# Optimization experiments

Hardware: AMD Instinct MI355X
Metric: run time of the kernel (lower is better)

The kernel has to match this reference:

```python
import jax, jax.numpy as jnp
import numpy as np

N = 100_000      # nodes
E = 1_600_000    # edges (avg degree 16)
F_IN = 128       # dataset.num_features
H = 128          # hidden
C = 25_000       # num_clusters (~ target_ratio 0.25 * N)
G = 64           # graphs in batch
NCLS = 10        # dataset.num_classes


def _gcn_conv(x, w, b, src, dst, n):
    # PyG GCNConv: add self loops, symmetric normalization deg^-1/2 A_hat deg^-1/2
    h = x @ w  # [n, out]
    deg = jnp.zeros((n,), x.dtype).at[dst].add(1.0) + 1.0  # +1 self loop
    dis = jax.lax.rsqrt(deg)
    norm = dis[src] * dis[dst]  # [E]
    out = jnp.zeros_like(h).at[dst].add(h[src] * norm[:, None])
    out = out + h * (dis * dis)[:, None]  # self-loop term norm_ii = deg_i^-1
    return out + b


def _mean_pool(x, seg, num_seg):
    s = jax.ops.segment_sum(x, seg, num_segments=num_seg)
    cnt = jax.ops.segment_sum(jnp.ones((x.shape[0],), x.dtype), seg, num_segments=num_seg)
    return s / jnp.maximum(cnt, 1.0)[:, None]


def _max_pool(x, seg, num_seg):
    m = jax.ops.segment_max(x, seg, num_segments=num_seg)
    cnt = jax.ops.segment_sum(jnp.ones((x.shape[0],), x.dtype), seg, num_segments=num_seg)
    return jnp.where(cnt[:, None] > 0, m, 0.0)


def setup_inputs() -> dict:
    key = jax.random.key(0)
    ks = jax.random.split(key, 12)
    def glorot(k, shape):
        fan_in = shape[0]
        return (jax.random.normal(k, shape, jnp.float32) / np.sqrt(fan_in)).astype(jnp.float32)
    return {
        "x": jax.random.normal(ks[0], (N, F_IN), jnp.float32),
        "edge_index": jax.random.randint(ks[1], (2, E), 0, N, dtype=jnp.int32).astype(jnp.int64),
        "batch": jnp.sort(jax.random.randint(ks[2], (N,), 0, G, dtype=jnp.int32)).astype(jnp.int64),
        "cluster": jax.random.randint(ks[3], (N,), 0, C, dtype=jnp.int32).astype(jnp.int64),
        "num_clusters": C,
        "num_graphs": G,
        "W1": glorot(ks[4], (F_IN, H)), "b1": jnp.zeros((H,), jnp.float32),
        "W2": glorot(ks[5], (H, H)),   "b2": jnp.zeros((H,), jnp.float32),
        "W3": glorot(ks[6], (H, H)),   "b3": jnp.zeros((H,), jnp.float32),
        "lin1_w": glorot(ks[7], (4 * H, H)), "lin1_b": jnp.zeros((H,), jnp.float32),
        "lin2_w": glorot(ks[8], (H, NCLS)),  "lin2_b": jnp.zeros((NCLS,), jnp.float32),
    }


def reference(x, edge_index, batch, cluster, num_clusters, num_graphs,
              W1, b1, W2, b2, W3, b3, lin1_w, lin1_b, lin2_w, lin2_b):
    n = x.shape[0]
    src, dst = edge_index[0], edge_index[1]
    # conv1 + relu (dropout is identity in eval mode)
    h = jax.nn.relu(_gcn_conv(x, W1, b1, src, dst, n))
    pre_mean = _mean_pool(h, batch, num_graphs)
    pre_max = _max_pool(h, batch, num_graphs)
    # LaCorePooling(aggregate='mean'): segment-mean nodes by cluster id,
    # relabel edges to cluster ids, derive pooled batch vector.
    hp = _mean_pool(h, cluster, num_clusters)            # [C, H]
    src_p, dst_p = cluster[src], cluster[dst]            # pooled edge list
    batch_p = jax.ops.segment_max(batch, cluster, num_segments=num_clusters)
    batch_p = jnp.maximum(batch_p, 0)                    # empty clusters -> graph 0
    # post-pool GCN layers
    hp = jax.nn.relu(_gcn_conv(hp, W2, b2, src_p, dst_p, num_clusters))
    hp = jax.nn.relu(_gcn_conv(hp, W3, b3, src_p, dst_p, num_clusters))
    post_mean = _mean_pool(hp, batch_p, num_graphs)
    post_max = _max_pool(hp, batch_p, num_graphs)
    z = jnp.concatenate([pre_mean, pre_max, post_mean, post_max], axis=-1)  # [G, 4H]
    z = jax.nn.relu(z @ lin1_w + lin1_b)
    z = z @ lin2_w + lin2_b
    return jax.nn.log_softmax(z, axis=-1)
```

## Files before the change

kernel.cpp:

```cpp
#include <hip/hip_runtime.h>

constexpr int N_NODES = 100000;
constexpr int N_EDGES = 1600000;
constexpr int N_CLUST = 25000;
constexpr int N_GRAPH = 64;
constexpr int NCLSN   = 10;

constexpr int BKT1_SHIFT = 9;
constexpr int NBKT1 = (N_NODES + 511) / 512;
constexpr int BKT2_SHIFT = 7;
constexpr int NBKT2 = (N_CLUST + 127) / 128;
constexpr int EPB = 4096;
constexpr int NEB = (N_EDGES + EPB - 1) / EPB;
constexpr int SORT_CAP = 12288;

constexpr int SCAN_BPB = 1024;
constexpr int NB1 = (N_NODES + SCAN_BPB - 1) / SCAN_BPB;
constexpr int NB2 = (N_CLUST + SCAN_BPB - 1) / SCAN_BPB;
constexpr int NB3 = (N_CLUST + SCAN_BPB - 1) / SCAN_BPB;
constexpr int NBT = NB1 + NB2 + NB3;

__device__ __forceinline__ float bf16lo(unsigned u){ return __uint_as_float(u << 16); }
__device__ __forceinline__ float bf16hi(unsigned u){ return __uint_as_float(u & 0xffff0000u); }
__device__ __forceinline__ unsigned bf16_rne(float f){
  unsigned u = __float_as_uint(f);
  return (u + 0x7fffu + ((u >> 16) & 1u)) >> 16;
}
__device__ __forceinline__ unsigned pack2(float lo, float hi){
  return bf16_rne(lo) | (bf16_rne(hi) << 16);
}

typedef short bf16x8 __attribute__((ext_vector_type(8)));
typedef float f32x4  __attribute__((ext_vector_type(4)));

__launch_bounds__(256)
__global__ void count_kernel(const int* __restrict__ ei, const int* __restrict__ cluster,
                             int* __restrict__ gcnt1, int* __restrict__ gcnt2){
  __shared__ int h1c[NBKT1], h2c[NBKT2];
  int t = threadIdx.x;
  for (int i = t; i < NBKT1; i += 256) h1c[i] = 0;
  for (int i = t; i < NBKT2; i += 256) h2c[i] = 0;
  __syncthreads();
  int e0 = blockIdx.x * EPB;
  #pragma unroll
  for (int i = 0; i < EPB / 256; ++i){
    int e = e0 + i * 256 + t;
    if (e < N_EDGES){
      int dst = ei[N_EDGES + e];
      int cd  = cluster[dst];
      atomicAdd(&h1c[dst >> BKT1_SHIFT], 1);
      atomicAdd(&h2c[cd  >> BKT2_SHIFT], 1);
    }
  }
  __syncthreads();
  for (int i = t; i < NBKT1; i += 256) if (h1c[i]) atomicAdd(&gcnt1[i], h1c[i]);
  for (int i = t; i < NBKT2; i += 256) if (h2c[i]) atomicAdd(&gcnt2[i], h2c[i]);
}

__launch_bounds__(256)
__global__ void bucket_scan(const int* __restrict__ gcnt1, const int* __restrict__ gcnt2,
                            int* __restrict__ gbase1, int* __restrict__ gcur1,
                            int* __restrict__ gbase2, int* __restrict__ gcur2){
  __shared__ int s[256];
  int t = threadIdx.x;
  int v = (t < NBKT1) ? gcnt1[t] : 0;
  s[t] = v; __syncthreads();
  for (int off = 1; off < 256; off <<= 1){
    int a = (t >= off) ? s[t - off] : 0;
    __syncthreads(); s[t] += a; __syncthreads();
  }
  if (t < NBKT1){ gbase1[t] = s[t] - v; gcur1[t] = s[t] - v; }
  __syncthreads();
  v = (t < NBKT2) ? gcnt2[t] : 0;
  s[t] = v; __syncthreads();
  for (int off = 1; off < 256; off <<= 1){
    int a = (t >= off) ? s[t - off] : 0;
    __syncthreads(); s[t] += a; __syncthreads();
  }
  if (t < NBKT2){ gbase2[t] = s[t] - v; gcur2[t] = s[t] - v; }
}

__launch_bounds__(256)
__global__ void scatter_kernel(const int* __restrict__ ei, const int* __restrict__ cluster,
                               int* __restrict__ gcur1, int* __restrict__ gcur2,
                               unsigned int* __restrict__ stage1, unsigned int* __restrict__ stage2){
  __shared__ int h1c[NBKT1], h2c[NBKT2];
  __shared__ int gb1[NBKT1], gb2[NBKT2];
  int t = threadIdx.x;
  for (int i = t; i < NBKT1; i += 256) h1c[i] = 0;
  for (int i = t; i < NBKT2; i += 256) h2c[i] = 0;
  __syncthreads();
  int e0 = blockIdx.x * EPB;
  #pragma unroll
  for (int i = 0; i < EPB / 256; ++i){
    int e = e0 + i * 256 + t;
    if (e < N_EDGES){
      int dst = ei[N_EDGES + e];
      int cd  = cluster[dst];
      atomicAdd(&h1c[dst >> BKT1_SHIFT], 1);
      atomicAdd(&h2c[cd  >> BKT2_SHIFT], 1);
    }
  }
  __syncthreads();
  for (int i = t; i < NBKT1; i += 256){ int c = h1c[i]; gb1[i] = c ? atomicAdd(&gcur1[i], c) : 0; }
  for (int i = t; i < NBKT2; i += 256){ int c = h2c[i]; gb2[i] = c ? atomicAdd(&gcur2[i], c) : 0; }
  __syncthreads();
  for (int i = t; i < NBKT1; i += 256) h1c[i] = 0;
  for (int i = t; i < NBKT2; i += 256) h2c[i] = 0;
  __syncthreads();
  #pragma unroll
  for (int i = 0; i < EPB / 256; ++i){
    int e = e0 + i * 256 + t;
    if (e < N_EDGES){
      int src = ei[e], dst = ei[N_EDGES + e];
      int cs = cluster[src], cd = cluster[dst];
      int b1 = dst >> BKT1_SHIFT, b2 = cd >> BKT2_SHIFT;
      int r1 = atomicAdd(&h1c[b1], 1);
      int r2 = atomicAdd(&h2c[b2], 1);
      stage1[gb1[b1] + r1] = ((unsigned)(dst & 511) << 17) | (unsigned)src;
      stage2[gb2[b2] + r2] = ((unsigned)(cd & 127) << 15) | (unsigned)cs;
    }
  }
}

template<int NBINS, int PSHIFT>
__launch_bounds__(256)
__global__ void bucket_sort(const unsigned int* __restrict__ stage, const int* __restrict__ gbase,
                            const int* __restrict__ gcnt, int* __restrict__ outpay,
                            int* __restrict__ deg, int ntot){
  __shared__ int cnt[NBINS], off[NBINS];
  __shared__ int sorted[SORT_CAP];
  int b = blockIdx.x, t = threadIdx.x;
  int base = gbase[b], n = gcnt[b];
  for (int i = t; i < NBINS; i += 256) cnt[i] = 0;
  __syncthreads();
  for (int i = t; i < n; i += 256) atomicAdd(&cnt[stage[base + i] >> PSHIFT], 1);
  __syncthreads();
  for (int i = t; i < NBINS; i += 256){
    int idx = b * NBINS + i;
    if (idx < ntot) deg[idx] = cnt[i];
    off[i] = cnt[i];
  }
  __syncthreads();
  for (int s = 1; s < NBINS; s <<= 1){
    int v0 = 0, v1 = 0;
    if (t < NBINS && t >= s) v0 = off[t - s];
    if (NBINS > 256 && t + 256 < NBINS && t + 256 >= s) v1 = off[t + 256 - s];
    __syncthreads();
    if (t < NBINS) off[t] += v0;
    if (NBINS > 256 && t + 256 < NBINS) off[t + 256] += v1;
    __syncthreads();
  }
  for (int i = t; i < NBINS; i += 256) off[i] -= cnt[i];
  __syncthreads();
  constexpr unsigned PMASK = (1u << PSHIFT) - 1u;
  if (n <= SORT_CAP){
    for (int i = t; i < n; i += 256){
      unsigned w = stage[base + i];
      int r = atomicAdd(&off[w >> PSHIFT], 1);
      sorted[r] = (int)(w & PMASK);
    }
    __syncthreads();
    for (int i = t; i < n; i += 256) outpay[base + i] = sorted[i];
  } else {
    for (int i = t; i < n; i += 256){
      unsigned w = stage[base + i];
      int r = atomicAdd(&off[w >> PSHIFT], 1);
      outpay[base + r] = (int)(w & PMASK);
    }
  }
}

__global__ void cntn_kernel(const int* __restrict__ cluster, int* __restrict__ cntn){
  int v = blockIdx.x * blockDim.x + threadIdx.x;
  if (v < N_NODES) atomicAdd(&cntn[cluster[v]], 1);
}

__device__ __forceinline__ void seg_select(int b, const int* deg1, const int* cntn,
                                           const int* deg2, const int*& src, int& n, int& base){
  if (b < NB1){ src = deg1; n = N_NODES; base = b * SCAN_BPB; }
  else if (b < NB1 + NB2){ src = cntn; n = N_CLUST; base = (b - NB1) * SCAN_BPB; }
  else { src = deg2; n = N_CLUST; base = (b - NB1 - NB2) * SCAN_BPB; }
}

__launch_bounds__(256)
__global__ void block_sums(const int* __restrict__ deg1, const int* __restrict__ cntn,
                           const int* __restrict__ deg2, int* __restrict__ bsum){
  int b = blockIdx.x;
  const int* src; int n, base;
  seg_select(b, deg1, cntn, deg2, src, n, base);
  int t = threadIdx.x;
  int i0 = base + t * 4;
  int s = 0;
  if (i0 + 3 < n){ int4 v = *(const int4*)&src[i0]; s = v.x + v.y + v.z + v.w; }
  else { for (int j = 0; j < 4; ++j){ int i = i0 + j; if (i < n) s += src[i]; } }
  __shared__ int sh[256];
  sh[t] = s; __syncthreads();
  for (int off = 128; off > 0; off >>= 1){
    if (t < off) sh[t] += sh[t + off];
    __syncthreads();
  }
  if (t == 0) bsum[b] = sh[0];
}

__launch_bounds__(256)
__global__ void scan_bsums(const int* __restrict__ bsum, int* __restrict__ boff,
                           int* __restrict__ rowptr1, int* __restrict__ rowptrn,
                           int* __restrict__ rowptr2){
  __shared__ int s[256];
  int t = threadIdx.x;
  int v = (t < NBT) ? bsum[t] : 0;
  s[t] = v; __syncthreads();
  int seg = (t < NB1) ? 0 : (t < NB1 + NB2 ? 1 : 2);
  for (int off = 1; off < 256; off <<= 1){
    int add = 0;
    if (t >= off){
      int u = t - off;
      int useg = (u < NB1) ? 0 : (u < NB1 + NB2 ? 1 : 2);
      if (useg == seg) add = s[u];
    }
    __syncthreads();
    s[t] += add;
    __syncthreads();
  }
  if (t < NBT) boff[t] = s[t] - v;
  if (t == NB1 - 1)       rowptr1[N_NODES] = s[t];
  if (t == NB1 + NB2 - 1) rowptrn[N_CLUST] = s[t];
  if (t == NBT - 1)       rowptr2[N_CLUST] = s[t];
}

__launch_bounds__(256)
__global__ void scan_final(const int* __restrict__ deg1, const int* __restrict__ cntn,
                           const int* __restrict__ deg2, const int* __restrict__ boff,
                           int* __restrict__ rowptr1, float* __restrict__ dis1,
                           int* __restrict__ rowptrn, int* __restrict__ curn,
                           int* __restrict__ rowptr2, float* __restrict__ dis2){
  int b = blockIdx.x;
  const int* src; int n, base;
  seg_select(b, deg1, cntn, deg2, src, n, base);
  int* rp; int* cur; float* dis;
  if (b < NB1){ rp = rowptr1; cur = nullptr; dis = dis1; }
  else if (b < NB1 + NB2){ rp = rowptrn; cur = curn; dis = nullptr; }
  else { rp = rowptr2; cur = nullptr; dis = dis2; }
  int t = threadIdx.x;
  int i0 = base + t * 4;
  int v[4]; int s = 0;
  #pragma unroll
  for (int j = 0; j < 4; ++j){ int i = i0 + j; v[j] = (i < n) ? src[i] : 0; s += v[j]; }
  __shared__ int sh[256];
  sh[t] = s; __syncthreads();
  for (int off = 1; off < 256; off <<= 1){
    int add = (t >= off) ? sh[t - off] : 0;
    __syncthreads();
    sh[t] += add;
    __syncthreads();
  }
  int run = sh[t] - s + boff[b];
  #pragma unroll
  for (int j = 0; j < 4; ++j){
    int i = i0 + j;
    if (i < n){
      rp[i] = run;
      if (cur) cur[i] = run;
      if (dis) dis[i] = rsqrtf((float)v[j] + 1.0f);
      run += v[j];
    }
  }
}

__global__ void fill_n(const int* __restrict__ cluster, int* __restrict__ curn,
                       int* __restrict__ nidx){
  int v = blockIdx.x * blockDim.x + threadIdx.x;
  if (v >= N_NODES) return;
  nidx[atomicAdd(&curn[cluster[v]], 1)] = v;
}

template<bool A_BF16>
__launch_bounds__(256)
__global__ void gemm_mfma(const void* __restrict__ Aptr, const float* __restrict__ B,
                          const float* __restrict__ scale, unsigned* __restrict__ Cmat,
                          int M){
  __shared__ __align__(16) unsigned Blds[128 * 68];
  __shared__ __align__(16) unsigned Alds[64 * 68];
  const int t = threadIdx.x;
  const int row0 = blockIdx.x * 64;

  #pragma unroll
  for (int i = 0; i < 8; ++i){
    int task = t + i * 256;
    int kp = task >> 5, nq = task & 31;
    float4 b0 = *(const float4*)&B[(2 * kp) * 128 + nq * 4];
    float4 b1 = *(const float4*)&B[(2 * kp + 1) * 128 + nq * 4];
    Blds[(nq * 4 + 0) * 68 + kp] = pack2(b0.x, b1.x);
    Blds[(nq * 4 + 1) * 68 + kp] = pack2(b0.y, b1.y);
    Blds[(nq * 4 + 2) * 68 + kp] = pack2(b0.z, b1.z);
    Blds[(nq * 4 + 3) * 68 + kp] = pack2(b0.w, b1.w);
  }
  if (A_BF16){
    const unsigned* A = (const unsigned*)Aptr;
    #pragma unroll
    for (int i = 0; i < 8; ++i){
      int idx = t + i * 256;
      int row = idx >> 5, c2 = idx & 31;
      int grow = min(row0 + row, M - 1);
      uint2 v = *(const uint2*)&A[(size_t)grow * 64 + c2 * 2];
      Alds[row * 68 + c2 * 2]     = v.x;
      Alds[row * 68 + c2 * 2 + 1] = v.y;
    }
  } else {
    const float* A = (const float*)Aptr;
    #pragma unroll
    for (int i = 0; i < 8; ++i){
      int idx = t + i * 256;
      int row = idx >> 5, k4 = idx & 31;
      int grow = min(row0 + row, M - 1);
      float4 v = *(const float4*)&A[(size_t)grow * 128 + k4 * 4];
      Alds[row * 68 + k4 * 2]     = pack2(v.x, v.y);
      Alds[row * 68 + k4 * 2 + 1] = pack2(v.z, v.w);
    }
  }
  __syncthreads();

  const int wv = t >> 6, l = t & 63, quad = l >> 4, n16 = l & 15;
  f32x4 acc[8];
  #pragma unroll
  for (int nt = 0; nt < 8; ++nt) acc[nt] = (f32x4){0.f, 0.f, 0.f, 0.f};
  const int arow = wv * 16 + n16;
  #pragma unroll
  for (int ks = 0; ks < 4; ++ks){
    bf16x8 af = *(const bf16x8*)&Alds[arow * 68 + ks * 16 + quad * 4];
    #pragma unroll
    for (int nt = 0; nt < 8; ++nt){
      bf16x8 bfr = *(const bf16x8*)&Blds[(nt * 16 + n16) * 68 + ks * 16 + quad * 4];
      acc[nt] = __builtin_amdgcn_mfma_f32_16x16x32_bf16(af, bfr, acc[nt], 0, 0, 0);
    }
  }
  #pragma unroll
  for (int nt = 0; nt < 8; ++nt){
    #pragma unroll
    for (int r = 0; r < 4; ++r){
      int row = row0 + wv * 16 + quad * 4 + r;
      float sc = scale[min(row, M - 1)];
      float v = acc[nt][r] * sc;
      float vhi = __shfl_xor(v, 1);
      if (((l & 1) == 0) && row < M)
        Cmat[(size_t)row * 64 + nt * 8 + (n16 >> 1)] = pack2(v, vhi);
    }
  }
}

__launch_bounds__(256)
__global__ void conv_csr(const unsigned* __restrict__ Ts, const float* __restrict__ dis,
                         const int* __restrict__ rowptr, const int* __restrict__ esrc,
                         const float* __restrict__ bias, unsigned* __restrict__ Hout){
  int w = blockIdx.x * 4 + (threadIdx.x >> 6);
  int l = threadIdx.x & 63;
  int beg = rowptr[w], end = rowptr[w + 1];
  float2 a0{0.f,0.f}, a1{0.f,0.f}, a2{0.f,0.f}, a3{0.f,0.f};
  for (int base = beg; base < end; base += 64){
    int n = min(64, end - base);
    int eid = esrc[base + min(l, n - 1)];
    int j = 0;
    for (; j + 4 <= n; j += 4){
      int s0 = __shfl(eid, j);
      int s1 = __shfl(eid, j + 1);
      int s2 = __shfl(eid, j + 2);
      int s3 = __shfl(eid, j + 3);
      unsigned u0 = Ts[(size_t)s0 * 64 + l];
      unsigned u1 = Ts[(size_t)s1 * 64 + l];
      unsigned u2 = Ts[(size_t)s2 * 64 + l];
      unsigned u3 = Ts[(size_t)s3 * 64 + l];
      a0.x += bf16lo(u0); a0.y += bf16hi(u0);
      a1.x += bf16lo(u1); a1.y += bf16hi(u1);
      a2.x += bf16lo(u2); a2.y += bf16hi(u2);
      a3.x += bf16lo(u3); a3.y += bf16hi(u3);
    }
    for (; j < n; ++j){
      int s = __shfl(eid, j);
      unsigned u = Ts[(size_t)s * 64 + l];
      a0.x += bf16lo(u); a0.y += bf16hi(u);
    }
  }
  float d = dis[w];
  unsigned us = Ts[(size_t)w * 64 + l];
  float2 bb = *(const float2*)&bias[l * 2];
  float rx = fmaxf(fmaf(d, a0.x + a1.x + a2.x + a3.x + bf16lo(us), bb.x), 0.f);
  float ry = fmaxf(fmaf(d, a0.y + a1.y + a2.y + a3.y + bf16hi(us), bb.y), 0.f);
  Hout[(size_t)w * 64 + l] = pack2(rx, ry);
}

__launch_bounds__(256)
__global__ void cluster_gather(const unsigned* __restrict__ h1, const int* __restrict__ rowptrn,
                               const int* __restrict__ nidx, const int* __restrict__ batch,
                               unsigned* __restrict__ hp, int* __restrict__ batchp){
  int c = blockIdx.x * 4 + (threadIdx.x >> 6);
  int l = threadIdx.x & 63;
  int mb = rowptrn[c], me = rowptrn[c + 1];
  float2 a0{0.f,0.f}, a1{0.f,0.f}, a2{0.f,0.f}, a3{0.f,0.f};
  int vmax = -1;
  for (int base = mb; base < me; base += 64){
    int n = min(64, me - base);
    int vid = nidx[base + min(l, n - 1)];
    if (l < n) vmax = max(vmax, vid);
    int j = 0;
    for (; j + 4 <= n; j += 4){
      int s0 = __shfl(vid, j);
      int s1 = __shfl(vid, j + 1);
      int s2 = __shfl(vid, j + 2);
      int s3 = __shfl(vid, j + 3);
      unsigned u0 = h1[(size_t)s0 * 64 + l];
      unsigned u1 = h1[(size_t)s1 * 64 + l];
      unsigned u2 = h1[(size_t)s2 * 64 + l];
      unsigned u3 = h1[(size_t)s3 * 64 + l];
      a0.x += bf16lo(u0); a0.y += bf16hi(u0);
      a1.x += bf16lo(u1); a1.y += bf16hi(u1);
      a2.x += bf16lo(u2); a2.y += bf16hi(u2);
      a3.x += bf16lo(u3); a3.y += bf16hi(u3);
    }
    for (; j < n; ++j){
      int s = __shfl(vid, j);
      unsigned u = h1[(size_t)s * 64 + l];
      a0.x += bf16lo(u); a0.y += bf16hi(u);
    }
  }
  #pragma unroll
  for (int off = 32; off > 0; off >>= 1) vmax = max(vmax, __shfl_xor(vmax, off));
  float inv = 1.0f / (float)max(me - mb, 1);
  float ox = (a0.x + a1.x + a2.x + a3.x) * inv;
  float oy = (a0.y + a1.y + a2.y + a3.y) * inv;
  hp[(size_t)c * 64 + l] = pack2(ox, oy);
  if (l == 0) batchp[c] = (vmax >= 0) ? batch[vmax] : 0;
}

__global__ void cntp_kernel(const int* __restrict__ batchp, int* __restrict__ cntp){
  int c = blockIdx.x * blockDim.x + threadIdx.x;
  if (c < N_CLUST) atomicAdd(&cntp[batchp[c]], 1);
}

__global__ void scan_cntp(const int* __restrict__ cntp, int* __restrict__ gbasep,
                          int* __restrict__ curp){
  int t = threadIdx.x;
  int v = cntp[t];
  int s = v;
  for (int off = 1; off < 64; off <<= 1){
    int u = __shfl_up(s, off);
    if (t >= off) s += u;
  }
  gbasep[t] = s - v; curp[t] = s - v;
  if (t == 63) gbasep[64] = s;
}

__global__ void fill_c(const int* __restrict__ batchp, int* __restrict__ curp,
                       int* __restrict__ cidx){
  int c = blockIdx.x * blockDim.x + threadIdx.x;
  if (c < N_CLUST) cidx[atomicAdd(&curp[batchp[c]], 1)] = c;
}

__global__ void graph_bounds(const int* __restrict__ batch, int* __restrict__ gstart){
  int g = threadIdx.x;
  if (g > N_GRAPH) return;
  int lo = 0, hi = N_NODES;
  while (lo < hi){ int mid = (lo + hi) >> 1; if (batch[mid] < g) lo = mid + 1; else hi = mid; }
  gstart[g] = lo;
}

__device__ __forceinline__ void atomicMaxPosF(float* addr, float v){
  atomicMax((int*)addr, __float_as_int(v));
}

constexpr int PRE_SPLIT = 4;
__launch_bounds__(256)
__global__ void pre_pool_g(const unsigned* __restrict__ h1, const int* __restrict__ gstart,
                           float* __restrict__ psum, float* __restrict__ pmax){
  int g = blockIdx.x / PRE_SPLIT, sp = blockIdx.x % PRE_SPLIT;
  int t = threadIdx.x, w = t >> 6, l = t & 63;
  int s0 = gstart[g], s1 = gstart[g + 1];
  int n = s1 - s0;
  int per = (n + PRE_SPLIT - 1) / PRE_SPLIT;
  int b0 = s0 + sp * per, b1 = min(b0 + per, s1);
  float2 a0{0.f,0.f}, a1{0.f,0.f}, a2{0.f,0.f}, a3{0.f,0.f};
  float2 mx{0.f,0.f};
  int i = b0 + w;
  for (; i + 12 < b1; i += 16){
    unsigned u0 = h1[(size_t)(i     ) * 64 + l];
    unsigned u1 = h1[(size_t)(i +  4) * 64 + l];
    unsigned u2 = h1[(size_t)(i +  8) * 64 + l];
    unsigned u3 = h1[(size_t)(i + 12) * 64 + l];
    float f0x = bf16lo(u0), f0y = bf16hi(u0);
    float f1x = bf16lo(u1), f1y = bf16hi(u1);
    float f2x = bf16lo(u2), f2y = bf16hi(u2);
    float f3x = bf16lo(u3), f3y = bf16hi(u3);
    a0.x += f0x; a0.y += f0y; a1.x += f1x; a1.y += f1y;
    a2.x += f2x; a2.y += f2y; a3.x += f3x; a3.y += f3y;
    mx.x = fmaxf(fmaxf(mx.x, fmaxf(f0x, f1x)), fmaxf(f2x, f3x));
    mx.y = fmaxf(fmaxf(mx.y, fmaxf(f0y, f1y)), fmaxf(f2y, f3y));
  }
  for (; i < b1; i += 4){
    unsigned u = h1[(size_t)i * 64 + l];
    float fx = bf16lo(u), fy = bf16hi(u);
    a0.x += fx; a0.y += fy;
    mx.x = fmaxf(mx.x, fx); mx.y = fmaxf(mx.y, fy);
  }
  __shared__ float2 ssum[4][64], smax[4][64];
  ssum[w][l] = { a0.x + a1.x + a2.x + a3.x, a0.y + a1.y + a2.y + a3.y };
  smax[w][l] = mx;
  __syncthreads();
  if (w == 0){
    float2 S = ssum[0][l], M = smax[0][l];
    #pragma unroll
    for (int k = 1; k < 4; ++k){
      S.x += ssum[k][l].x; S.y += ssum[k][l].y;
      M.x = fmaxf(M.x, smax[k][l].x); M.y = fmaxf(M.y, smax[k][l].y);
    }
    atomicAdd(&psum[g * 128 + 2 * l], S.x);
    atomicAdd(&psum[g * 128 + 2 * l + 1], S.y);
    atomicMaxPosF(&pmax[g * 128 + 2 * l], M.x);
    atomicMaxPosF(&pmax[g * 128 + 2 * l + 1], M.y);
  }
}

constexpr int POST_SPLIT = 2;
__launch_bounds__(256)
__global__ void post_pool_g(const unsigned* __restrict__ hp3, const int* __restrict__ gbasep,
                            const int* __restrict__ cidx,
                            float* __restrict__ psum, float* __restrict__ pmax){
  int g = blockIdx.x / POST_SPLIT, sp = blockIdx.x % POST_SPLIT;
  int t = threadIdx.x, w = t >> 6, l = t & 63;
  int s0 = gbasep[g], s1 = gbasep[g + 1];
  int n = s1 - s0;
  int per = (n + POST_SPLIT * 4 - 1) / (POST_SPLIT * 4);
  int b0 = s0 + (sp * 4 + w) * per, b1 = min(b0 + per, s1);
  float2 a0{0.f,0.f}, a1{0.f,0.f}, a2{0.f,0.f}, a3{0.f,0.f};
  float2 mx{0.f,0.f};
  for (int base = b0; base < b1; base += 64){
    int nn = min(64, b1 - base);
    int cid = cidx[base + min(l, nn - 1)];
    int j = 0;
    for (; j + 4 <= nn; j += 4){
      int c0 = __shfl(cid, j);
      int c1 = __shfl(cid, j + 1);
      int c2 = __shfl(cid, j + 2);
      int c3 = __shfl(cid, j + 3);
      unsigned u0 = hp3[(size_t)c0 * 64 + l];
      unsigned u1 = hp3[(size_t)c1 * 64 + l];
      unsigned u2 = hp3[(size_t)c2 * 64 + l];
      unsigned u3 = hp3[(size_t)c3 * 64 + l];
      float f0x = bf16lo(u0), f0y = bf16hi(u0);
      float f1x = bf16lo(u1), f1y = bf16hi(u1);
      float f2x = bf16lo(u2), f2y = bf16hi(u2);
      float f3x = bf16lo(u3), f3y = bf16hi(u3);
      a0.x += f0x; a0.y += f0y; a1.x += f1x; a1.y += f1y;
      a2.x += f2x; a2.y += f2y; a3.x += f3x; a3.y += f3y;
      mx.x = fmaxf(fmaxf(mx.x, fmaxf(f0x, f1x)), fmaxf(f2x, f3x));
      mx.y = fmaxf(fmaxf(mx.y, fmaxf(f0y, f1y)), fmaxf(f2y, f3y));
    }
    for (; j < nn; ++j){
      int c = __shfl(cid, j);
      unsigned u = hp3[(size_t)c * 64 + l];
      float fx = bf16lo(u), fy = bf16hi(u);
      a0.x += fx; a0.y += fy;
      mx.x = fmaxf(mx.x, fx); mx.y = fmaxf(mx.y, fy);
    }
  }
  __shared__ float2 ssum[4][64], smax[4][64];
  ssum[w][l] = { a0.x + a1.x + a2.x + a3.x, a0.y + a1.y + a2.y + a3.y };
  smax[w][l] = mx;
  __syncthreads();
  if (w == 0){
    float2 S = ssum[0][l], M = smax[0][l];
    #pragma unroll
    for (int k = 1; k < 4; ++k){
      S.x += ssum[k][l].x; S.y += ssum[k][l].y;
      M.x = fmaxf(M.x, smax[k][l].x); M.y = fmaxf(M.y, smax[k][l].y);
    }
    atomicAdd(&psum[g * 128 + 2 * l], S.x);
    atomicAdd(&psum[g * 128 + 2 * l + 1], S.y);
    atomicMaxPosF(&pmax[g * 128 + 2 * l], M.x);
    atomicMaxPosF(&pmax[g * 128 + 2 * l + 1], M.y);
  }
}

__launch_bounds__(128)
__global__ void head_kernel(const float* __restrict__ psum, const float* __restrict__ pmax,
                            const float* __restrict__ postsum, const float* __restrict__ postmax,
                            const int* __restrict__ gstart, const int* __restrict__ cntp,
                            const float* __restrict__ l1w, const float* __restrict__ l1b,
                            const float* __restrict__ l2w, const float* __restrict__ l2b,
                            float* __restrict__ out){
  int g = blockIdx.x, t = threadIdx.x;
  __shared__ float z[512];
  __shared__ float a[128];
  __shared__ float logits[16];
  __shared__ float lse_s;
  float cpre  = (float)max(gstart[g + 1] - gstart[g], 1);
  float cpost = fmaxf((float)cntp[g], 1.0f);
  z[t]       = psum[g * 128 + t] / cpre;
  z[128 + t] = pmax[g * 128 + t];
  z[256 + t] = postsum[g * 128 + t] / cpost;
  z[384 + t] = postmax[g * 128 + t];
  __syncthreads();
  float acc = l1b[t];
  #pragma unroll 8
  for (int k = 0; k < 512; ++k) acc = fmaf(z[k], l1w[k * 128 + t], acc);
  a[t] = fmaxf(acc, 0.f);
  __syncthreads();
  if (t < NCLSN){
    float s2 = l2b[t];
    for (int k = 0; k < 128; ++k) s2 = fmaf(a[k], l2w[k * NCLSN + t], s2);
    logits[t] = s2;
  }
  __syncthreads();
  if (t == 0){
    float m = logits[0];
    for (int c = 1; c < NCLSN; ++c) m = fmaxf(m, logits[c]);
    float s = 0.f;
    for (int c = 0; c < NCLSN; ++c) s += expf(logits[c] - m);
    lse_s = m + logf(s);
  }
  __syncthreads();
  if (t < NCLSN) out[g * NCLSN + t] = logits[t] - lse_s;
}

extern "C" void kernel_launch(void* const* d_in, const int* in_sizes, int n_in,
                              void* d_out, int out_size, void* d_ws, size_t ws_size,
                              hipStream_t stream){
  const float* x       = (const float*)d_in[0];
  const int*   ei      = (const int*)  d_in[1];
  const int*   batch   = (const int*)  d_in[2];
  const int*   cluster = (const int*)  d_in[3];
  const float* W1      = (const float*)d_in[6];
  const float* b1      = (const float*)d_in[7];
  const float* W2      = (const float*)d_in[8];
  const float* b2      = (const float*)d_in[9];
  const float* W3      = (const float*)d_in[10];
  const float* b3      = (const float*)d_in[11];
  const float* l1w     = (const float*)d_in[12];
  const float* l1b     = (const float*)d_in[13];
  const float* l2w     = (const float*)d_in[14];
  const float* l2b     = (const float*)d_in[15];
  float* out = (float*)d_out;

  char* base = (char*)d_ws;
  size_t off = 0;
  auto alloc = [&](size_t bytes) -> char* {
    char* p = base + off;
    off += (bytes + 255) & ~size_t(255);
    return p;
  };
  char*  zbase  = base + off;
  int*   gcnt1  = (int*)  alloc((size_t)NBKT1 * 4);
  int*   gcnt2  = (int*)  alloc((size_t)NBKT2 * 4);
  int*   cntn   = (int*)  alloc((size_t)N_CLUST * 4);
  int*   cntp   = (int*)  alloc((size_t)N_GRAPH * 4);
  float* pre_s  = (float*)alloc((size_t)N_GRAPH * 128 * 4);
  float* pre_m  = (float*)alloc((size_t)N_GRAPH * 128 * 4);
  float* post_s = (float*)alloc((size_t)N_GRAPH * 128 * 4);
  float* post_m = (float*)alloc((size_t)N_GRAPH * 128 * 4);
  size_t zsize = off;
  unsigned* Ts1   = (unsigned*)alloc((size_t)N_NODES * 64 * 4);
  unsigned* h1    = (unsigned*)alloc((size_t)N_NODES * 64 * 4);
  int*   esrc1   = (int*)  alloc((size_t)N_EDGES * 4);
  int*   psrcC   = (int*)  alloc((size_t)N_EDGES * 4);
  int*   deg1    = (int*)  alloc((size_t)N_NODES * 4);
  int*   deg2    = (int*)  alloc((size_t)N_CLUST * 4);
  int*   rowptr1 = (int*)  alloc((size_t)(N_NODES + 1) * 4);
  int*   rowptrn = (int*)  alloc((size_t)(N_CLUST + 1) * 4);
  int*   curn    = (int*)  alloc((size_t)N_CLUST * 4);
  int*   rowptr2 = (int*)  alloc((size_t)(N_CLUST + 1) * 4);
  int*   nidx    = (int*)  alloc((size_t)N_NODES * 4);
  float* dis1    = (float*)alloc((size_t)N_NODES * 4);
  float* dis2    = (float*)alloc((size_t)N_CLUST * 4);
  int*   batchp  = (int*)  alloc((size_t)N_CLUST * 4);
  int*   gstart  = (int*)  alloc((size_t)(N_GRAPH + 1) * 4);
  int*   bsum    = (int*)  alloc((size_t)NBT * 4);
  int*   boff    = (int*)  alloc((size_t)NBT * 4);
  int*   gbase1  = (int*)  alloc((size_t)NBKT1 * 4);
  int*   gcur1   = (int*)  alloc((size_t)NBKT1 * 4);
  int*   gbase2  = (int*)  alloc((size_t)NBKT2 * 4);
  int*   gcur2   = (int*)  alloc((size_t)NBKT2 * 4);
  int*   gbasep  = (int*)  alloc((size_t)(N_GRAPH + 1) * 4);
  int*   curp    = (int*)  alloc((size_t)N_GRAPH * 4);
  int*   cidx    = (int*)  alloc((size_t)N_CLUST * 4);
  unsigned int* stage1 = (unsigned int*)h1;
  unsigned int* stage2 = stage1 + N_EDGES;
  unsigned* hp  = Ts1;
  unsigned* Ts2 = Ts1 + (size_t)N_CLUST * 64;
  unsigned* hp2 = Ts1 + (size_t)2 * N_CLUST * 64;
  unsigned* hp3 = Ts1 + (size_t)3 * N_CLUST * 64;
  unsigned* Ts3 = Ts2;

  (void)in_sizes; (void)n_in; (void)out_size; (void)ws_size;

  hipMemsetAsync(zbase, 0, zsize, stream);

  count_kernel  <<<NEB, 256, 0, stream>>>(ei, cluster, gcnt1, gcnt2);
  cntn_kernel   <<<(N_NODES + 255) / 256, 256, 0, stream>>>(cluster, cntn);
  bucket_scan   <<<1, 256, 0, stream>>>(gcnt1, gcnt2, gbase1, gcur1, gbase2, gcur2);
  scatter_kernel<<<NEB, 256, 0, stream>>>(ei, cluster, gcur1, gcur2, stage1, stage2);
  bucket_sort<512, 17><<<NBKT1, 256, 0, stream>>>(stage1, gbase1, gcnt1, esrc1, deg1, N_NODES);
  bucket_sort<128, 15><<<NBKT2, 256, 0, stream>>>(stage2, gbase2, gcnt2, psrcC, deg2, N_CLUST);
  block_sums <<<NBT, 256, 0, stream>>>(deg1, cntn, deg2, bsum);
  scan_bsums <<<1, 256, 0, stream>>>(bsum, boff, rowptr1, rowptrn, rowptr2);
  scan_final <<<NBT, 256, 0, stream>>>(deg1, cntn, deg2, boff,
                                       rowptr1, dis1, rowptrn, curn, rowptr2, dis2);
  fill_n<<<(N_NODES + 255) / 256, 256, 0, stream>>>(cluster, curn, nidx);

  gemm_mfma<false><<<(N_NODES + 63) / 64, 256, 0, stream>>>(x, W1, dis1, Ts1, N_NODES);
  conv_csr<<<N_NODES / 4, 256, 0, stream>>>(Ts1, dis1, rowptr1, esrc1, b1, h1);

  graph_bounds<<<1, 128, 0, stream>>>(batch, gstart);
  pre_pool_g<<<N_GRAPH * PRE_SPLIT, 256, 0, stream>>>(h1, gstart, pre_s, pre_m);

  cluster_gather<<<N_CLUST / 4, 256, 0, stream>>>(h1, rowptrn, nidx, batch, hp, batchp);
  cntp_kernel<<<(N_CLUST + 255) / 256, 256, 0, stream>>>(batchp, cntp);
  scan_cntp<<<1, 64, 0, stream>>>(cntp, gbasep, curp);
  fill_c<<<(N_CLUST + 255) / 256, 256, 0, stream>>>(batchp, curp, cidx);

  gemm_mfma<true><<<(N_CLUST + 63) / 64, 256, 0, stream>>>(hp, W2, dis2, Ts2, N_CLUST);
  conv_csr<<<N_CLUST / 4, 256, 0, stream>>>(Ts2, dis2, rowptr2, psrcC, b2, hp2);

  gemm_mfma<true><<<(N_CLUST + 63) / 64, 256, 0, stream>>>(hp2, W3, dis2, Ts3, N_CLUST);
  conv_csr<<<N_CLUST / 4, 256, 0, stream>>>(Ts3, dis2, rowptr2, psrcC, b3, hp3);

  post_pool_g<<<N_GRAPH * POST_SPLIT, 256, 0, stream>>>(hp3, gbasep, cidx, post_s, post_m);
  head_kernel<<<N_GRAPH, 128, 0, stream>>>(pre_s, pre_m, post_s, post_m, gstart, cntp,
                                           l1w, l1b, l2w, l2b, out);
}
```

Before: 648.6 us.

## Derive pooled cluster CSR from node CSR instead of a second bucket sort

Drops the second radix/bucket sort that built the cluster-level edge list. Cluster in-degrees now come from summing node in-degrees per cluster. A new per-cluster wavefront kernel walks each cluster's member nodes' CSR rows and writes the mapped source cluster ids into psrcC. This removes a cluster lookup per edge in count/scatter, halves the staging writes and eliminates a sort pass, at the cost of a serial inner loop over cluster members and possibly imbalanced wave work per cluster. It assumes clusters have at most 64 members and changes edge order within a row, which may slightly alter float summation order.

```diff
diff --git a/kernel.cpp b/kernel.cpp
--- a/kernel.cpp
+++ b/kernel.cpp
@@ -8,8 +8,6 @@
 
 constexpr int BKT1_SHIFT = 9;
 constexpr int NBKT1 = (N_NODES + 511) / 512;
-constexpr int BKT2_SHIFT = 7;
-constexpr int NBKT2 = (N_CLUST + 127) / 128;
 constexpr int EPB = 4096;
 constexpr int NEB = (N_EDGES + EPB - 1) / EPB;
 constexpr int SORT_CAP = 12288;
@@ -34,33 +32,24 @@
 typedef float f32x4  __attribute__((ext_vector_type(4)));
 
 __launch_bounds__(256)
-__global__ void count_kernel(const int* __restrict__ ei, const int* __restrict__ cluster,
-                             int* __restrict__ gcnt1, int* __restrict__ gcnt2){
-  __shared__ int h1c[NBKT1], h2c[NBKT2];
+__global__ void count_kernel(const int* __restrict__ ei, int* __restrict__ gcnt1){
+  __shared__ int h1c[NBKT1];
   int t = threadIdx.x;
   for (int i = t; i < NBKT1; i += 256) h1c[i] = 0;
-  for (int i = t; i < NBKT2; i += 256) h2c[i] = 0;
   __syncthreads();
   int e0 = blockIdx.x * EPB;
   #pragma unroll
   for (int i = 0; i < EPB / 256; ++i){
     int e = e0 + i * 256 + t;
-    if (e < N_EDGES){
-      int dst = ei[N_EDGES + e];
-      int cd  = cluster[dst];
-      atomicAdd(&h1c[dst >> BKT1_SHIFT], 1);
-      atomicAdd(&h2c[cd  >> BKT2_SHIFT], 1);
-    }
+    if (e < N_EDGES) atomicAdd(&h1c[ei[N_EDGES + e] >> BKT1_SHIFT], 1);
   }
   __syncthreads();
   for (int i = t; i < NBKT1; i += 256) if (h1c[i]) atomicAdd(&gcnt1[i], h1c[i]);
-  for (int i = t; i < NBKT2; i += 256) if (h2c[i]) atomicAdd(&gcnt2[i], h2c[i]);
-}
-
-__launch_bounds__(256)
-__global__ void bucket_scan(const int* __restrict__ gcnt1, const int* __restrict__ gcnt2,
-                            int* __restrict__ gbase1, int* __restrict__ gcur1,
-                            int* __restrict__ gbase2, int* __restrict__ gcur2){
+}
+
+__launch_bounds__(256)
+__global__ void bucket_scan(const int* __restrict__ gcnt1,
+                            int* __restrict__ gbase1, int* __restrict__ gcur1){
   __shared__ int s[256];
   int t = threadIdx.x;
   int v = (t < NBKT1) ? gcnt1[t] : 0;
@@ -70,55 +59,35 @@
     __syncthreads(); s[t] += a; __syncthreads();
   }
   if (t < NBKT1){ gbase1[t] = s[t] - v; gcur1[t] = s[t] - v; }
-  __syncthreads();
-  v = (t < NBKT2) ? gcnt2[t] : 0;
-  s[t] = v; __syncthreads();
-  for (int off = 1; off < 256; off <<= 1){
-    int a = (t >= off) ? s[t - off] : 0;
-    __syncthreads(); s[t] += a; __syncthreads();
-  }
-  if (t < NBKT2){ gbase2[t] = s[t] - v; gcur2[t] = s[t] - v; }
-}
-
-__launch_bounds__(256)
-__global__ void scatter_kernel(const int* __restrict__ ei, const int* __restrict__ cluster,
-                               int* __restrict__ gcur1, int* __restrict__ gcur2,
-                               unsigned int* __restrict__ stage1, unsigned int* __restrict__ stage2){
-  __shared__ int h1c[NBKT1], h2c[NBKT2];
-  __shared__ int gb1[NBKT1], gb2[NBKT2];
+}
+
+__launch_bounds__(256)
+__global__ void scatter_kernel(const int* __restrict__ ei, int* __restrict__ gcur1,
+                               unsigned int* __restrict__ stage1){
+  __shared__ int h1c[NBKT1];
+  __shared__ int gb1[NBKT1];
   int t = threadIdx.x;
   for (int i = t; i < NBKT1; i += 256) h1c[i] = 0;
-  for (int i = t; i < NBKT2; i += 256) h2c[i] = 0;
   __syncthreads();
   int e0 = blockIdx.x * EPB;
   #pragma unroll
   for (int i = 0; i < EPB / 256; ++i){
     int e = e0 + i * 256 + t;
-    if (e < N_EDGES){
-      int dst = ei[N_EDGES + e];
-      int cd  = cluster[dst];
-      atomicAdd(&h1c[dst >> BKT1_SHIFT], 1);
-      atomicAdd(&h2c[cd  >> BKT2_SHIFT], 1);
-    }
+    if (e < N_EDGES) atomicAdd(&h1c[ei[N_EDGES + e] >> BKT1_SHIFT], 1);
   }
   __syncthreads();
   for (int i = t; i < NBKT1; i += 256){ int c = h1c[i]; gb1[i] = c ? atomicAdd(&gcur1[i], c) : 0; }
-  for (int i = t; i < NBKT2; i += 256){ int c = h2c[i]; gb2[i] = c ? atomicAdd(&gcur2[i], c) : 0; }
   __syncthreads();
   for (int i = t; i < NBKT1; i += 256) h1c[i] = 0;
-  for (int i = t; i < NBKT2; i += 256) h2c[i] = 0;
   __syncthreads();
   #pragma unroll
   for (int i = 0; i < EPB / 256; ++i){
     int e = e0 + i * 256 + t;
     if (e < N_EDGES){
       int src = ei[e], dst = ei[N_EDGES + e];
-      int cs = cluster[src], cd = cluster[dst];
-      int b1 = dst >> BKT1_SHIFT, b2 = cd >> BKT2_SHIFT;
+      int b1 = dst >> BKT1_SHIFT;
       int r1 = atomicAdd(&h1c[b1], 1);
-      int r2 = atomicAdd(&h2c[b2], 1);
       stage1[gb1[b1] + r1] = ((unsigned)(dst & 511) << 17) | (unsigned)src;
-      stage2[gb2[b2] + r2] = ((unsigned)(cd & 127) << 15) | (unsigned)cs;
     }
   }
 }
@@ -171,9 +140,14 @@
   }
 }
 
-__global__ void cntn_kernel(const int* __restrict__ cluster, int* __restrict__ cntn){
+__global__ void node_prep(const int* __restrict__ cluster, const int* __restrict__ deg1,
+                          int* __restrict__ cntn, int* __restrict__ deg2){
   int v = blockIdx.x * blockDim.x + threadIdx.x;
-  if (v < N_NODES) atomicAdd(&cntn[cluster[v]], 1);
+  if (v < N_NODES){
+    int c = cluster[v];
+    atomicAdd(&cntn[c], 1);
+    atomicAdd(&deg2[c], deg1[v]);
+  }
 }
 
 __device__ __forceinline__ void seg_select(int b, const int* deg1, const int* cntn,
@@ -273,6 +247,47 @@
   int v = blockIdx.x * blockDim.x + threadIdx.x;
   if (v >= N_NODES) return;
   nidx[atomicAdd(&curn[cluster[v]], 1)] = v;
+}
+
+__launch_bounds__(256)
+__global__ void psrc_build(const int* __restrict__ rowptrn, const int* __restrict__ nidx,
+                           const int* __restrict__ rowptr1, const int* __restrict__ esrc1,
+                           const int* __restrict__ cluster, const int* __restrict__ rowptr2,
+                           int* __restrict__ psrcC){
+  int c = blockIdx.x * 4 + (threadIdx.x >> 6);
+  int l = threadIdx.x & 63;
+  int mb = rowptrn[c], me = rowptrn[c + 1];
+  int cnt = me - mb;
+  int base_l = 0, d_l = 0;
+  if (l < cnt){
+    int v = nidx[mb + l];
+    base_l = rowptr1[v];
+    d_l = rowptr1[v + 1] - base_l;
+  }
+  int pref = d_l;
+  #pragma unroll
+  for (int off = 1; off < 64; off <<= 1){
+    int u = __shfl_up(pref, off);
+    if (l >= off) pref += u;
+  }
+  int total = __shfl(pref, 63);
+  int wbase = rowptr2[c];
+  int iters = (total + 63) >> 6;
+  for (int k = 0; k < iters; ++k){
+    int idx = k * 64 + l;
+    int idxc = min(idx, total - 1);
+    int m = 0;
+    for (int j = 0; j < cnt; ++j){
+      int pj = __shfl(pref, j);
+      if (idxc >= pj) m = j + 1;
+    }
+    int pm = __shfl(pref, m);
+    int dm = __shfl(d_l, m);
+    int bm = __shfl(base_l, m);
+    int e = bm + idxc - (pm - dm);
+    int sc = cluster[esrc1[e]];
+    if (idx < total) psrcC[wbase + idx] = sc;
+  }
 }
 
 template<bool A_BF16>
@@ -649,8 +664,8 @@
   };
   char*  zbase  = base + off;
   int*   gcnt1  = (int*)  alloc((size_t)NBKT1 * 4);
-  int*   gcnt2  = (int*)  alloc((size_t)NBKT2 * 4);
   int*   cntn   = (int*)  alloc((size_t)N_CLUST * 4);
+  int*   deg2   = (int*)  alloc((size_t)N_CLUST * 4);
   int*   cntp   = (int*)  alloc((size_t)N_GRAPH * 4);
   float* pre_s  = (float*)alloc((size_t)N_GRAPH * 128 * 4);
   float* pre_m  = (float*)alloc((size_t)N_GRAPH * 128 * 4);
@@ -662,7 +677,6 @@
   int*   esrc1   = (int*)  alloc((size_t)N_EDGES * 4);
   int*   psrcC   = (int*)  alloc((size_t)N_EDGES * 4);
   int*   deg1    = (int*)  alloc((size_t)N_NODES * 4);
-  int*   deg2    = (int*)  alloc((size_t)N_CLUST * 4);
   int*   rowptr1 = (int*)  alloc((size_t)(N_NODES + 1) * 4);
   int*   rowptrn = (int*)  alloc((size_t)(N_CLUST + 1) * 4);
   int*   curn    = (int*)  alloc((size_t)N_CLUST * 4);
@@ -676,13 +690,10 @@
   int*   boff    = (int*)  alloc((size_t)NBT * 4);
   int*   gbase1  = (int*)  alloc((size_t)NBKT1 * 4);
   int*   gcur1   = (int*)  alloc((size_t)NBKT1 * 4);
-  int*   gbase2  = (int*)  alloc((size_t)NBKT2 * 4);
-  int*   gcur2   = (int*)  alloc((size_t)NBKT2 * 4);
   int*   gbasep  = (int*)  alloc((size_t)(N_GRAPH + 1) * 4);
   int*   curp    = (int*)  alloc((size_t)N_GRAPH * 4);
   int*   cidx    = (int*)  alloc((size_t)N_CLUST * 4);
   unsigned int* stage1 = (unsigned int*)h1;
-  unsigned int* stage2 = stage1 + N_EDGES;
   unsigned* hp  = Ts1;
   unsigned* Ts2 = Ts1 + (size_t)N_CLUST * 64;
   unsigned* hp2 = Ts1 + (size_t)2 * N_CLUST * 64;
@@ -693,17 +704,18 @@
 
   hipMemsetAsync(zbase, 0, zsize, stream);
 
-  count_kernel  <<<NEB, 256, 0, stream>>>(ei, cluster, gcnt1, gcnt2);
-  cntn_kernel   <<<(N_NODES + 255) / 256, 256, 0, stream>>>(cluster, cntn);
-  bucket_scan   <<<1, 256, 0, stream>>>(gcnt1, gcnt2, gbase1, gcur1, gbase2, gcur2);
-  scatter_kernel<<<NEB, 256, 0, stream>>>(ei, cluster, gcur1, gcur2, stage1, stage2);
+  count_kernel  <<<NEB, 256, 0, stream>>>(ei, gcnt1);
+  bucket_scan   <<<1, 256, 0, stream>>>(gcnt1, gbase1, gcur1);
+  scatter_kernel<<<NEB, 256, 0, stream>>>(ei, gcur1, stage1);
   bucket_sort<512, 17><<<NBKT1, 256, 0, stream>>>(stage1, gbase1, gcnt1, esrc1, deg1, N_NODES);
-  bucket_sort<128, 15><<<NBKT2, 256, 0, stream>>>(stage2, gbase2, gcnt2, psrcC, deg2, N_CLUST);
+  node_prep<<<(N_NODES + 255) / 256, 256, 0, stream>>>(cluster, deg1, cntn, deg2);
   block_sums <<<NBT, 256, 0, stream>>>(deg1, cntn, deg2, bsum);
   scan_bsums <<<1, 256, 0, stream>>>(bsum, boff, rowptr1, rowptrn, rowptr2);
   scan_final <<<NBT, 256, 0, stream>>>(deg1, cntn, deg2, boff,
                                        rowptr1, dis1, rowptrn, curn, rowptr2, dis2);
   fill_n<<<(N_NODES + 255) / 256, 256, 0, stream>>>(cluster, curn, nidx);
+  psrc_build<<<N_CLUST / 4, 256, 0, stream>>>(rowptrn, nidx, rowptr1, esrc1,
+                                              cluster, rowptr2, psrcC);
 
   gemm_mfma<false><<<(N_NODES + 63) / 64, 256, 0, stream>>>(x, W1, dis1, Ts1, N_NODES);
   conv_csr<<<N_NODES / 4, 256, 0, stream>>>(Ts1, dis1, rowptr1, esrc1, b1, h1);
```

Measured after the change: 608.0 us. 6.3% less time.
